# Kernel tuning notes

Measured on AMD Instinct MI355X. Metric: run time of the kernel, lower is better.

Reference implementation:

```python
import jax, jax.numpy as jnp
import numpy as np

N_USERS = 100000
N_GAMES = 20000
D_USER = 128
D_GAME = 64
EMB = 64
H = 256
E = 1000000
S = 500000


def setup_inputs() -> dict:
    key = jax.random.key(0)
    ks = jax.random.split(key, 32)

    def w(k, fi, fo):
        return jax.random.normal(k, (fi, fo), jnp.float32) / np.float32(np.sqrt(fi))

    d_game_full = D_GAME + EMB  # game features concat game embedding
    inp = {
        "x_user": jax.random.normal(ks[0], (N_USERS, D_USER), jnp.float32),
        "x_game": jax.random.normal(ks[1], (N_GAMES, D_GAME), jnp.float32),
        "emb_game": jax.random.normal(ks[2], (N_GAMES, EMB), jnp.float32) * 0.1,
        "edge_weight_ug": jax.random.uniform(ks[3], (E,), jnp.float32),
        "edge_weight_gu": jax.random.uniform(ks[4], (E,), jnp.float32),
        "src_ug": jax.random.randint(ks[5], (E,), 0, N_USERS, jnp.int32),
        "dst_ug": jax.random.randint(ks[6], (E,), 0, N_GAMES, jnp.int32),
        "src_gu": jax.random.randint(ks[7], (E,), 0, N_GAMES, jnp.int32),
        "dst_gu": jax.random.randint(ks[8], (E,), 0, N_USERS, jnp.int32),
        "score_row": jax.random.randint(ks[9], (S,), 0, N_USERS, jnp.int32),
        "score_col": jax.random.randint(ks[10], (S,), 0, N_GAMES, jnp.int32),
    }
    # GraphConv params per layer per edge type: W_rel (messages), bias, W_root (self)
    dims = [(D_USER, d_game_full, H), (H, H, H), (H, H, H)]
    i = 11
    for l, (du, dg, out) in enumerate(dims, 1):
        inp[f"W_rel_ug{l}"] = w(ks[i], du, out); i += 1
        inp[f"b_ug{l}"] = jnp.zeros((out,), jnp.float32)
        inp[f"W_root_g{l}"] = w(ks[i], dg, out); i += 1
        inp[f"W_rel_gu{l}"] = w(ks[i], dg, out); i += 1
        inp[f"b_gu{l}"] = jnp.zeros((out,), jnp.float32)
        inp[f"W_root_u{l}"] = w(ks[i], du, out); i += 1
    return inp


def reference(x_user, x_game, emb_game, edge_weight_ug, edge_weight_gu,
              W_rel_ug1, b_ug1, W_root_g1, W_rel_gu1, b_gu1, W_root_u1,
              W_rel_ug2, b_ug2, W_root_g2, W_rel_gu2, b_gu2, W_root_u2,
              W_rel_ug3, b_ug3, W_root_g3, W_rel_gu3, b_gu3, W_root_u3,
              src_ug, dst_ug, src_gu, dst_gu, score_row, score_col):
    def conv(x_src, x_dst, src, dst, ew, Wr, br, Wo, n_dst):
        # GraphConv: sum_j w_ij * x_j -> lin_rel, plus lin_root(x_i)
        msg = jax.ops.segment_sum(x_src[src] * ew[:, None], dst, num_segments=n_dst)
        return msg @ Wr + br + x_dst @ Wo

    xu = x_user                                   # [Nu, 128]
    xg = jnp.concatenate([x_game, emb_game], axis=1)  # [Ng, 128]

    g = jax.nn.relu(conv(xu, xg, src_ug, dst_ug, edge_weight_ug, W_rel_ug1, b_ug1, W_root_g1, N_GAMES))
    u = jax.nn.relu(conv(xg, xu, src_gu, dst_gu, edge_weight_gu, W_rel_gu1, b_gu1, W_root_u1, N_USERS))

    g2 = jax.nn.relu(conv(u, g, src_ug, dst_ug, edge_weight_ug, W_rel_ug2, b_ug2, W_root_g2, N_GAMES))
    u2 = jax.nn.relu(conv(g, u, src_gu, dst_gu, edge_weight_gu, W_rel_gu2, b_gu2, W_root_u2, N_USERS))

    g3 = conv(u2, g2, src_ug, dst_ug, edge_weight_ug, W_rel_ug3, b_ug3, W_root_g3, N_GAMES)
    u3 = conv(g2, u2, src_gu, dst_gu, edge_weight_gu, W_rel_gu3, b_gu3, W_root_u3, N_USERS)
    # dropout(0.2) in eval mode is identity

    # DotProductEdgeDecoder
    return jnp.sum(u3[score_row] * g3[score_col], axis=1)  # [S]
```

## Files before the change

kernel.cpp:

```cpp
#include <hip/hip_runtime.h>

typedef unsigned short bf16_t;
typedef __attribute__((ext_vector_type(8))) short bf16x8;
typedef __attribute__((ext_vector_type(4))) float f32x4;

static constexpr int NU = 100000;
static constexpr int NG = 20000;
static constexpr int HD = 256;
static constexpr int EE = 1000000;
static constexpr int SS = 500000;

static constexpr int SPAN = 1024;
static constexpr int BKT_G = (NG + SPAN - 1) / SPAN;
static constexpr int BKT_U = (NU + SPAN - 1) / SPAN;
static constexpr int PA_BLOCKS = 128;
static constexpr int PA_CHUNK = (EE + PA_BLOCKS - 1) / PA_BLOCKS;
static constexpr int TILE = 4096;

__device__ __forceinline__ float b2f(bf16_t u) {
    union { unsigned int i; float f; } x; x.i = ((unsigned int)u) << 16; return x.f;
}
__device__ __forceinline__ bf16_t f2b(float f) {
    union { float f; unsigned int i; } x; x.f = f;
    unsigned int r = x.i + 0x7FFF + ((x.i >> 16) & 1);
    return (bf16_t)(r >> 16);
}

__device__ __forceinline__ void accum8(float* acc, uint4 r, float w) {
    unsigned int u[4] = {r.x, r.y, r.z, r.w};
#pragma unroll
    for (int i = 0; i < 4; i++) {
        float lo = __uint_as_float(u[i] << 16);
        float hi = __uint_as_float(u[i] & 0xFFFF0000u);
        acc[2 * i]     = fmaf(w, lo, acc[2 * i]);
        acc[2 * i + 1] = fmaf(w, hi, acc[2 * i + 1]);
    }
}

__global__ void prep_feats(const float* __restrict__ xgame, const float* __restrict__ emb,
                           const float* __restrict__ xuser,
                           bf16_t* __restrict__ xg, bf16_t* __restrict__ xu,
                           int* __restrict__ gcg, int* __restrict__ gcu) {
    int id = blockIdx.x * 256 + threadIdx.x;
    if (id < BKT_G) gcg[id] = 0;
    if (id < BKT_U) gcu[id] = 0;
    const int ng4 = NG * 32;
    if (id < ng4) {
        int r = id >> 5, c = (id & 31) * 4;
        float4 v = (c < 64) ? *(const float4*)&xgame[(size_t)r * 64 + c]
                            : *(const float4*)&emb[(size_t)r * 64 + (c - 64)];
        ((ushort4*)xg)[id] = make_ushort4(f2b(v.x), f2b(v.y), f2b(v.z), f2b(v.w));
    } else {
        int j = id - ng4;
        if (j >= NU * 32) return;
        float4 v = ((const float4*)xuser)[j];
        ((ushort4*)xu)[j] = make_ushort4(f2b(v.x), f2b(v.y), f2b(v.z), f2b(v.w));
    }
}

struct WtArgs {
    const float* src[12];
    bf16_t* dst[12];
    int K[12];
    int off[13];
};
__global__ void wt_all(WtArgs a, int total) {
    int id = blockIdx.x * 256 + threadIdx.x;
    if (id >= total) return;
    int s = 0;
    while (id >= a.off[s + 1]) ++s;
    int local = id - a.off[s];
    int K = a.K[s];
    int k = local >> 8, n = local & 255;
    a.dst[s][(size_t)n * K + k] = f2b(a.src[s][local]);
}

__global__ __launch_bounds__(256) void chisto(const int* __restrict__ dug,
                                              const int* __restrict__ dgu,
                                              int* __restrict__ gcg, int* __restrict__ gcu) {
    __shared__ int cnt[128];
    int blk = blockIdx.x;
    int dir = blk >> 7, lb = blk & 127;
    const int* dst = dir ? dgu : dug;
    int* gc = dir ? gcu : gcg;
    int B = dir ? BKT_U : BKT_G;
    int t = threadIdx.x;
    if (t < 128) cnt[t] = 0;
    __syncthreads();
    int beg = lb * PA_CHUNK, fin = min(EE, beg + PA_CHUNK);
    for (int i = beg + t; i < fin; i += 256)
        atomicAdd(&cnt[((unsigned)dst[i]) >> 10], 1);
    __syncthreads();
    if (t < B && cnt[t]) atomicAdd(&gc[t], cnt[t]);
}

__global__ void scan_coarse(const int* __restrict__ gcg, const int* __restrict__ gcu,
                            int* __restrict__ baseg, int* __restrict__ baseu,
                            int* __restrict__ gcurg, int* __restrict__ gcuru,
                            int* __restrict__ rpg, int* __restrict__ rpu) {
    if (blockIdx.x == 0 && threadIdx.x == 0) {
        int run = 0;
        for (int i = 0; i < BKT_G; i++) { baseg[i] = run; gcurg[i] = run; run += gcg[i]; }
        rpg[NG] = EE;
    } else if (blockIdx.x == 1 && threadIdx.x == 0) {
        int run = 0;
        for (int i = 0; i < BKT_U; i++) { baseu[i] = run; gcuru[i] = run; run += gcu[i]; }
        rpu[NU] = EE;
    }
}

__global__ __launch_bounds__(256) void passA(
    const int* __restrict__ sug, const int* __restrict__ dug, const float* __restrict__ wug,
    const int* __restrict__ sgu, const int* __restrict__ dgu, const float* __restrict__ wgu,
    int* __restrict__ gcurg, int* __restrict__ gcuru,
    int2* __restrict__ tmpG, int2* __restrict__ tmpU) {
    __shared__ int cnt[128], sscan[128], gb[128];
    __shared__ unsigned short rankArr[TILE];
    __shared__ unsigned char sbkt[TILE];
    __shared__ int2 staged[TILE];
    int blk = blockIdx.x;
    int dir = blk >> 7, lb = blk & 127;
    const int* src = dir ? sgu : sug;
    const int* dst = dir ? dgu : dug;
    const float* w = dir ? wgu : wug;
    int* gcur = dir ? gcuru : gcurg;
    int2* tmp = dir ? tmpU : tmpG;
    int B = dir ? BKT_U : BKT_G;
    int t = threadIdx.x;
    int beg = lb * PA_CHUNK, fin = min(EE, beg + PA_CHUNK);
    for (int tb = beg; tb < fin; tb += TILE) {
        int n = min(TILE, fin - tb);
        if (t < 128) cnt[t] = 0;
        __syncthreads();
        for (int i = t; i < n; i += 256) {
            int bkt = ((unsigned)dst[tb + i]) >> 10;
            rankArr[i] = (unsigned short)atomicAdd(&cnt[bkt], 1);
        }
        __syncthreads();
        if (t == 0) {
            int run = 0;
            for (int i = 0; i < 128; i++) { sscan[i] = run; run += cnt[i]; }
        }
        __syncthreads();
        for (int i = t; i < n; i += 256) {
            unsigned d = (unsigned)dst[tb + i];
            int bkt = d >> 10;
            int pos = sscan[bkt] + rankArr[i];
            staged[pos] = make_int2(src[tb + i] | ((d & 1023u) << 17), __float_as_int(w[tb + i]));
            sbkt[pos] = (unsigned char)bkt;
        }
        __syncthreads();
        if (t < B && cnt[t]) gb[t] = atomicAdd(&gcur[t], cnt[t]);
        __syncthreads();
        for (int i = t; i < n; i += 256) {
            int bkt = sbkt[i];
            tmp[gb[bkt] + i - sscan[bkt]] = staged[i];
        }
        __syncthreads();
    }
}

__global__ __launch_bounds__(256) void passB(
    const int2* __restrict__ tmpG, const int2* __restrict__ tmpU,
    const int* __restrict__ baseg, const int* __restrict__ baseu,
    int* __restrict__ rpg, int* __restrict__ rpu,
    int2* __restrict__ eug, int2* __restrict__ egu) {
    __shared__ int hist[SPAN], excl[SPAN], sd[256];
    int b = blockIdx.x;
    const int2* tmp; const int* base; int* rowptr; int2* eout; int bkt, B, ntot;
    if (b < BKT_G) { tmp = tmpG; base = baseg; rowptr = rpg; eout = eug; bkt = b; B = BKT_G; ntot = NG; }
    else           { tmp = tmpU; base = baseu; rowptr = rpu; eout = egu; bkt = b - BKT_G; B = BKT_U; ntot = NU; }
    int start = base[bkt];
    int end = (bkt == B - 1) ? EE : base[bkt + 1];
    int row0 = bkt * SPAN;
    int t = threadIdx.x;
    for (int i = t; i < SPAN; i += 256) hist[i] = 0;
    __syncthreads();
    for (int i = start + t; i < end; i += 256)
        atomicAdd(&hist[((unsigned)tmp[i].x) >> 17], 1);
    __syncthreads();
    int v[4]; int s = 0;
#pragma unroll
    for (int j = 0; j < 4; j++) { v[j] = hist[t * 4 + j]; s += v[j]; }
    sd[t] = s;
    __syncthreads();
    for (int off = 1; off < 256; off <<= 1) {
        int y = (t >= off) ? sd[t - off] : 0;
        __syncthreads();
        sd[t] += y;
        __syncthreads();
    }
    int run = sd[t] - s;
#pragma unroll
    for (int j = 0; j < 4; j++) { excl[t * 4 + j] = run; run += v[j]; }
    __syncthreads();
    for (int r = t; r < SPAN; r += 256) {
        int row = row0 + r;
        if (row < ntot) rowptr[row] = start + excl[r];
    }
    for (int i = t; i < SPAN; i += 256) hist[i] = 0;
    __syncthreads();
    for (int i = start + t; i < end; i += 256) {
        int2 e = tmp[i];
        int dl = ((unsigned)e.x) >> 17;
        int pos = start + excl[dl] + atomicAdd(&hist[dl], 1);
        eout[pos] = make_int2(e.x & 0x1FFFF, e.y);
    }
}

template <int D>
__global__ __launch_bounds__(256) void seg_sum16(
    const bf16_t* __restrict__ feat, const int* __restrict__ rowptr,
    const int2* __restrict__ edges, bf16_t* __restrict__ out, int n_rows) {
    constexpr int LPE = D / 8;
    constexpr int EP = 64 / LPE;
    constexpr int UN = 4;
    int wid = (blockIdx.x * 256 + threadIdx.x) >> 6;
    int lane = threadIdx.x & 63;
    if (wid >= n_rows) return;
    int beg = rowptr[wid], end = rowptr[wid + 1];
    const int h = lane / LPE;
    const int cl = lane % LPE;
    const uint4* fb = (const uint4*)feat;
    float acc[8] = {};
    for (int eb = beg; eb < end; eb += UN * EP) {
        int2 ed[UN]; bool v[UN]; uint4 r[UN];
#pragma unroll
        for (int u = 0; u < UN; u++) {
            int e = eb + u * EP + h;
            v[u] = e < end;
            ed[u] = edges[v[u] ? e : beg];
        }
#pragma unroll
        for (int u = 0; u < UN; u++)
            r[u] = fb[(size_t)ed[u].x * (D / 8) + cl];
#pragma unroll
        for (int u = 0; u < UN; u++)
            accum8(acc, r[u], v[u] ? __int_as_float(ed[u].y) : 0.f);
    }
#pragma unroll
    for (int k = 0; k < 8; ++k) {
        acc[k] += __shfl_down(acc[k], 32, 64);
        if (LPE == 16) acc[k] += __shfl_down(acc[k], 16, 64);
    }
    if (lane < LPE) {
        uint4 o;
        o.x = (unsigned)f2b(acc[0]) | ((unsigned)f2b(acc[1]) << 16);
        o.y = (unsigned)f2b(acc[2]) | ((unsigned)f2b(acc[3]) << 16);
        o.z = (unsigned)f2b(acc[4]) | ((unsigned)f2b(acc[5]) << 16);
        o.w = (unsigned)f2b(acc[6]) | ((unsigned)f2b(acc[7]) << 16);
        ((uint4*)(out + (size_t)wid * D))[lane] = o;
    }
}

template <bool TWOPASS>
__global__ __launch_bounds__(256) void gemm_mfma(
    const bf16_t* __restrict__ A1, const bf16_t* __restrict__ W1t,
    const bf16_t* __restrict__ A2, const bf16_t* __restrict__ W2t,
    const float* __restrict__ bias, bf16_t* __restrict__ C,
    int M, int K, int addc, int relu) {
    constexpr int LS = 40;
    __shared__ bf16_t As[128 * LS];
    __shared__ bf16_t Bs[128 * LS];
    const int t = threadIdx.x;
    const int lane = t & 63, wave = t >> 6;
    const int wm = (wave >> 1) * 64, wn = (wave & 1) * 64;
    const int rowBase = blockIdx.x * 128;
    const int colBase = blockIdx.y * 128;
    const int lm = lane & 15;
    const int quad = lane >> 4;
    f32x4 acc[4][4] = {};

    const int npass = TWOPASS ? 2 : 1;
    for (int pass = 0; pass < npass; ++pass) {
        const bf16_t* A = pass ? A2 : A1;
        const bf16_t* Wt = pass ? W2t : W1t;
        for (int k0 = 0; k0 < K; k0 += 32) {
#pragma unroll
            for (int i = 0; i < 2; ++i) {
                int li = t + i * 256;
                int r = li >> 2, c = (li & 3) * 8;
                int gm = rowBase + r;
                bf16x8 v = {};
                if (gm < M) v = *(const bf16x8*)&A[(size_t)gm * K + k0 + c];
                *(bf16x8*)&As[r * LS + c] = v;
            }
#pragma unroll
            for (int i = 0; i < 2; ++i) {
                int li = t + i * 256;
                int r = li >> 2, c = (li & 3) * 8;
                bf16x8 v = *(const bf16x8*)&Wt[(size_t)(colBase + r) * K + k0 + c];
                *(bf16x8*)&Bs[r * LS + c] = v;
            }
            __syncthreads();
            bf16x8 af[4], bfr[4];
#pragma unroll
            for (int i = 0; i < 4; ++i)
                af[i] = *(const bf16x8*)&As[(wm + i * 16 + lm) * LS + quad * 8];
#pragma unroll
            for (int j = 0; j < 4; ++j)
                bfr[j] = *(const bf16x8*)&Bs[(wn + j * 16 + lm) * LS + quad * 8];
#pragma unroll
            for (int i = 0; i < 4; ++i)
#pragma unroll
                for (int j = 0; j < 4; ++j)
                    acc[i][j] = __builtin_amdgcn_mfma_f32_16x16x32_bf16(af[i], bfr[j], acc[i][j], 0, 0, 0);
            __syncthreads();
        }
    }

#pragma unroll
    for (int j = 0; j < 4; ++j) {
        int col = colBase + wn + j * 16 + lm;
        float bj = bias ? bias[col] : 0.f;
#pragma unroll
        for (int i = 0; i < 4; ++i) {
            int row0 = rowBase + wm + i * 16 + quad * 4;
#pragma unroll
            for (int r = 0; r < 4; ++r) {
                int row = row0 + r;
                if (row >= M) continue;
                float v = acc[i][j][r] + bj;
                bf16_t* cp = &C[(size_t)row * HD + col];
                if (addc) v += b2f(*cp);
                if (relu) v = fmaxf(v, 0.f);
                *cp = f2b(v);
            }
        }
    }
}

__global__ __launch_bounds__(256) void decode2(
    const bf16_t* __restrict__ u3, const bf16_t* __restrict__ g3,
    const int* __restrict__ row, const int* __restrict__ col,
    float* __restrict__ out, int S) {
    int wid = (blockIdx.x * 256 + threadIdx.x) >> 6;
    int lane = threadIdx.x & 63;
    int p = wid * 2 + (lane >> 5);
    int cl = lane & 31;
    if (p >= S) p = S - 1;
    int r = row[p], c = col[p];
    uint4 a = ((const uint4*)(u3 + (size_t)r * 256))[cl];
    uint4 b = ((const uint4*)(g3 + (size_t)c * 256))[cl];
    float s = 0.f;
    unsigned ua[4] = {a.x, a.y, a.z, a.w}, ub[4] = {b.x, b.y, b.z, b.w};
#pragma unroll
    for (int i = 0; i < 4; i++) {
        float alo = __uint_as_float(ua[i] << 16), ahi = __uint_as_float(ua[i] & 0xFFFF0000u);
        float blo = __uint_as_float(ub[i] << 16), bhi = __uint_as_float(ub[i] & 0xFFFF0000u);
        s = fmaf(alo, blo, s);
        s = fmaf(ahi, bhi, s);
    }
#pragma unroll
    for (int d = 16; d > 0; d >>= 1) s += __shfl_down(s, d, 64);
    if (cl == 0) out[p] = s;
}

extern "C" void kernel_launch(void* const* d_in, const int* in_sizes, int n_in,
                              void* d_out, int out_size, void* d_ws, size_t ws_size,
                              hipStream_t stream) {
    const float* x_user  = (const float*)d_in[0];
    const float* x_game  = (const float*)d_in[1];
    const float* emb_game= (const float*)d_in[2];
    const float* ew_ug   = (const float*)d_in[3];
    const float* ew_gu   = (const float*)d_in[4];
    const int* src_ug    = (const int*)d_in[5];
    const int* dst_ug    = (const int*)d_in[6];
    const int* src_gu    = (const int*)d_in[7];
    const int* dst_gu    = (const int*)d_in[8];
    const int* score_row = (const int*)d_in[9];
    const int* score_col = (const int*)d_in[10];
    const float* Wr_ug[3] = {(const float*)d_in[11], (const float*)d_in[17], (const float*)d_in[23]};
    const float* b_ug[3]  = {(const float*)d_in[12], (const float*)d_in[18], (const float*)d_in[24]};
    const float* Wo_g[3]  = {(const float*)d_in[13], (const float*)d_in[19], (const float*)d_in[25]};
    const float* Wr_gu[3] = {(const float*)d_in[14], (const float*)d_in[20], (const float*)d_in[26]};
    const float* b_gu[3]  = {(const float*)d_in[15], (const float*)d_in[21], (const float*)d_in[27]};
    const float* Wo_u[3]  = {(const float*)d_in[16], (const float*)d_in[22], (const float*)d_in[28]};
    float* out = (float*)d_out;
    (void)in_sizes; (void)n_in; (void)out_size;

    constexpr size_t WS_NEEDED = 183500000;
    if (ws_size < WS_NEEDED) return;

    char* ws = (char*)d_ws;
    size_t off = 0;
    auto alloc = [&](size_t bytes) -> void* {
        void* p = ws + off;
        off += (bytes + 255) & ~(size_t)255;
        return p;
    };
    bf16_t* xg   = (bf16_t*)alloc((size_t)NG * 128 * 2);
    bf16_t* xu   = (bf16_t*)alloc((size_t)NU * 128 * 2);
    bf16_t* uA   = (bf16_t*)alloc((size_t)NU * HD * 2);
    bf16_t* uB   = (bf16_t*)alloc((size_t)NU * HD * 2);
    bf16_t* gA   = (bf16_t*)alloc((size_t)NG * HD * 2);
    bf16_t* gB   = (bf16_t*)alloc((size_t)NG * HD * 2);
    bf16_t* buf  = (bf16_t*)alloc((size_t)NG * HD * 2);
    int2*   e_ug = (int2*)  alloc((size_t)EE * 8);
    int2*   e_gu = (int2*)  alloc((size_t)EE * 8);
    bf16_t* WrugT[3], *WogT[3], *WrguT[3], *WouT[3];
    const int Ks[3] = {128, 256, 256};
    for (int l = 0; l < 3; ++l) {
        WrugT[l] = (bf16_t*)alloc((size_t)Ks[l] * HD * 2);
        WogT[l]  = (bf16_t*)alloc((size_t)Ks[l] * HD * 2);
        WrguT[l] = (bf16_t*)alloc((size_t)Ks[l] * HD * 2);
        WouT[l]  = (bf16_t*)alloc((size_t)Ks[l] * HD * 2);
    }
    int* rowptr_g = (int*)alloc((NG + 1) * 4);
    int* rowptr_u = (int*)alloc((NU + 1) * 4);
    int* gcnt_g   = (int*)alloc(BKT_G * 4);
    int* gcnt_u   = (int*)alloc(BKT_U * 4);
    int* base_g   = (int*)alloc(BKT_G * 4);
    int* base_u   = (int*)alloc(BKT_U * 4);
    int* gcur_g   = (int*)alloc(BKT_G * 4);
    int* gcur_u   = (int*)alloc(BKT_U * 4);
    int2* tmp_g = (int2*)uB;
    int2* tmp_u = tmp_g + EE;

    {
        int n4 = NG * 32 + NU * 32;
        prep_feats<<<(n4 + 255) / 256, 256, 0, stream>>>(x_game, emb_game, x_user, xg, xu,
                                                         gcnt_g, gcnt_u);
        WtArgs wa;
        const float* srcs[12] = {Wr_ug[0], Wo_g[0], Wr_gu[0], Wo_u[0],
                                 Wr_ug[1], Wo_g[1], Wr_gu[1], Wo_u[1],
                                 Wr_ug[2], Wo_g[2], Wr_gu[2], Wo_u[2]};
        bf16_t* dsts[12] = {WrugT[0], WogT[0], WrguT[0], WouT[0],
                            WrugT[1], WogT[1], WrguT[1], WouT[1],
                            WrugT[2], WogT[2], WrguT[2], WouT[2]};
        int total = 0;
        for (int i = 0; i < 12; ++i) {
            wa.src[i] = srcs[i]; wa.dst[i] = dsts[i];
            wa.K[i] = Ks[i / 4]; wa.off[i] = total;
            total += Ks[i / 4] * HD;
        }
        wa.off[12] = total;
        wt_all<<<(total + 255) / 256, 256, 0, stream>>>(wa, total);
    }
    chisto<<<2 * PA_BLOCKS, 256, 0, stream>>>(dst_ug, dst_gu, gcnt_g, gcnt_u);
    scan_coarse<<<2, 64, 0, stream>>>(gcnt_g, gcnt_u, base_g, base_u, gcur_g, gcur_u,
                                      rowptr_g, rowptr_u);
    passA<<<2 * PA_BLOCKS, 256, 0, stream>>>(src_ug, dst_ug, ew_ug, src_gu, dst_gu, ew_gu,
                                             gcur_g, gcur_u, tmp_g, tmp_u);
    passB<<<BKT_G + BKT_U, 256, 0, stream>>>(tmp_g, tmp_u, base_g, base_u,
                                             rowptr_g, rowptr_u, e_ug, e_gu);

    const dim3 GG((NG + 127) / 128, 2), GU((NU + 127) / 128, 2);
    const int SEG_G = (NG + 3) / 4, SEG_U = (NU + 3) / 4;

    seg_sum16<128><<<SEG_G, 256, 0, stream>>>(xu, rowptr_g, e_ug, buf, NG);
    gemm_mfma<true><<<GG, 256, 0, stream>>>(buf, WrugT[0], xg, WogT[0], b_ug[0], gA, NG, 128, 0, 1);
    gemm_mfma<false><<<GG, 256, 0, stream>>>(xg, WrguT[0], nullptr, nullptr, nullptr, buf, NG, 128, 0, 0);
    seg_sum16<256><<<SEG_U, 256, 0, stream>>>(buf, rowptr_u, e_gu, uA, NU);
    gemm_mfma<false><<<GU, 256, 0, stream>>>(xu, WouT[0], nullptr, nullptr, b_gu[0], uA, NU, 128, 1, 1);

    seg_sum16<256><<<SEG_G, 256, 0, stream>>>(uA, rowptr_g, e_ug, buf, NG);
    gemm_mfma<true><<<GG, 256, 0, stream>>>(buf, WrugT[1], gA, WogT[1], b_ug[1], gB, NG, 256, 0, 1);
    gemm_mfma<false><<<GG, 256, 0, stream>>>(gA, WrguT[1], nullptr, nullptr, nullptr, buf, NG, 256, 0, 0);
    seg_sum16<256><<<SEG_U, 256, 0, stream>>>(buf, rowptr_u, e_gu, uB, NU);
    gemm_mfma<false><<<GU, 256, 0, stream>>>(uA, WouT[1], nullptr, nullptr, b_gu[1], uB, NU, 256, 1, 1);

    seg_sum16<256><<<SEG_G, 256, 0, stream>>>(uB, rowptr_g, e_ug, buf, NG);
    gemm_mfma<true><<<GG, 256, 0, stream>>>(buf, WrugT[2], gB, WogT[2], b_ug[2], gA, NG, 256, 0, 0);
    gemm_mfma<false><<<GG, 256, 0, stream>>>(gB, WrguT[2], nullptr, nullptr, nullptr, buf, NG, 256, 0, 0);
    seg_sum16<256><<<SEG_U, 256, 0, stream>>>(buf, rowptr_u, e_gu, uA, NU);
    gemm_mfma<false><<<GU, 256, 0, stream>>>(uB, WouT[2], nullptr, nullptr, b_gu[2], uA, NU, 256, 1, 0);

    decode2<<<((SS + 1) / 2 + 3) / 4, 256, 0, stream>>>(uA, gA, score_row, score_col, out, SS);
}
```

Baseline: 1.128 ms.

## Split CSR fine-sort pass into sliced histogram, global scan, and atomic scatter

The per-bucket fine sort, which ran one block per 1024-row bucket (118 blocks total), is replaced by a sliced global-histogram pass (8 blocks per bucket), a three-kernel global prefix scan over per-row counts, and a scatter pass that uses global atomics on per-row cursors. The coarse pass block count is also doubled. The aim is more parallelism in the CSR build, paid for with extra kernel launches, global atomics and additional count and cursor arrays. Edge order within a row becomes nondeterministic, which can change the summation order.

New measurement: 1.100 ms. -2.5%, faster.

```diff
diff --git a/kernel.cpp b/kernel.cpp
--- a/kernel.cpp
+++ b/kernel.cpp
@@ -13,9 +13,11 @@
 static constexpr int SPAN = 1024;
 static constexpr int BKT_G = (NG + SPAN - 1) / SPAN;
 static constexpr int BKT_U = (NU + SPAN - 1) / SPAN;
-static constexpr int PA_BLOCKS = 128;
+static constexpr int PA_BLOCKS = 256;
 static constexpr int PA_CHUNK = (EE + PA_BLOCKS - 1) / PA_BLOCKS;
 static constexpr int TILE = 4096;
+static constexpr int NSC_G = (NG + 1023) / 1024;
+static constexpr int NSC_U = (NU + 1023) / 1024;
 
 __device__ __forceinline__ float b2f(bf16_t u) {
     union { unsigned int i; float f; } x; x.i = ((unsigned int)u) << 16; return x.f;
@@ -77,10 +79,14 @@
 
 __global__ __launch_bounds__(256) void chisto(const int* __restrict__ dug,
                                               const int* __restrict__ dgu,
-                                              int* __restrict__ gcg, int* __restrict__ gcu) {
+                                              int* __restrict__ gcg, int* __restrict__ gcu,
+                                              int* __restrict__ rcg, int* __restrict__ rcu) {
     __shared__ int cnt[128];
     int blk = blockIdx.x;
-    int dir = blk >> 7, lb = blk & 127;
+    int gid = blk * 256 + threadIdx.x;
+    if (gid < NG) rcg[gid] = 0;
+    else if (gid < NG + NU) rcu[gid - NG] = 0;
+    int dir = blk >> 8, lb = blk & 255;
     const int* dst = dir ? dgu : dug;
     int* gc = dir ? gcu : gcg;
     int B = dir ? BKT_U : BKT_G;
@@ -119,7 +125,7 @@
     __shared__ unsigned char sbkt[TILE];
     __shared__ int2 staged[TILE];
     int blk = blockIdx.x;
-    int dir = blk >> 7, lb = blk & 127;
+    int dir = blk >> 8, lb = blk & 255;
     const int* src = dir ? sgu : sug;
     const int* dst = dir ? dgu : dug;
     const float* w = dir ? wgu : wug;
@@ -160,28 +166,50 @@
     }
 }
 
-__global__ __launch_bounds__(256) void passB(
+__device__ __forceinline__ void slice_bounds(const int* base, int bkt, int B, int sl,
+                                             int& s0, int& s1) {
+    int start = base[bkt];
+    int end = (bkt == B - 1) ? EE : base[bkt + 1];
+    int len = end - start;
+    s0 = start + (int)(((long long)len * sl) >> 3);
+    s1 = start + (int)(((long long)len * (sl + 1)) >> 3);
+}
+
+__global__ __launch_bounds__(256) void passB_hist(
     const int2* __restrict__ tmpG, const int2* __restrict__ tmpU,
     const int* __restrict__ baseg, const int* __restrict__ baseu,
-    int* __restrict__ rpg, int* __restrict__ rpu,
-    int2* __restrict__ eug, int2* __restrict__ egu) {
-    __shared__ int hist[SPAN], excl[SPAN], sd[256];
-    int b = blockIdx.x;
-    const int2* tmp; const int* base; int* rowptr; int2* eout; int bkt, B, ntot;
-    if (b < BKT_G) { tmp = tmpG; base = baseg; rowptr = rpg; eout = eug; bkt = b; B = BKT_G; ntot = NG; }
-    else           { tmp = tmpU; base = baseu; rowptr = rpu; eout = egu; bkt = b - BKT_G; B = BKT_U; ntot = NU; }
-    int start = base[bkt];
-    int end = (bkt == B - 1) ? EE : base[bkt + 1];
-    int row0 = bkt * SPAN;
+    int* __restrict__ rcg, int* __restrict__ rcu) {
+    __shared__ int hist[SPAN];
+    int b = blockIdx.x >> 3, sl = blockIdx.x & 7;
+    const int2* tmp; const int* base; int* rowcnt; int bkt, B;
+    if (b < BKT_G) { tmp = tmpG; base = baseg; rowcnt = rcg; bkt = b; B = BKT_G; }
+    else           { tmp = tmpU; base = baseu; rowcnt = rcu; bkt = b - BKT_G; B = BKT_U; }
+    int s0, s1;
+    slice_bounds(base, bkt, B, sl, s0, s1);
     int t = threadIdx.x;
     for (int i = t; i < SPAN; i += 256) hist[i] = 0;
     __syncthreads();
-    for (int i = start + t; i < end; i += 256)
+    for (int i = s0 + t; i < s1; i += 256)
         atomicAdd(&hist[((unsigned)tmp[i].x) >> 17], 1);
     __syncthreads();
+    int row0 = bkt * SPAN;
+    for (int i = t; i < SPAN; i += 256)
+        if (hist[i]) atomicAdd(&rowcnt[row0 + i], hist[i]);
+}
+
+__device__ __forceinline__ void scan1_body(const int* cnt, int* rowptr, int* bsum,
+                                           int* cur, int n, int lb) {
+    __shared__ int sd[256];
+    int t = threadIdx.x;
+    int base = lb * 1024;
     int v[4]; int s = 0;
 #pragma unroll
-    for (int j = 0; j < 4; j++) { v[j] = hist[t * 4 + j]; s += v[j]; }
+    for (int i = 0; i < 4; i++) {
+        int idx = base + t * 4 + i;
+        v[i] = (idx < n) ? cnt[idx] : 0;
+        if (idx < n) cur[idx] = 0;
+        s += v[i];
+    }
     sd[t] = s;
     __syncthreads();
     for (int off = 1; off < 256; off <<= 1) {
@@ -192,18 +220,74 @@
     }
     int run = sd[t] - s;
 #pragma unroll
-    for (int j = 0; j < 4; j++) { excl[t * 4 + j] = run; run += v[j]; }
-    __syncthreads();
-    for (int r = t; r < SPAN; r += 256) {
-        int row = row0 + r;
-        if (row < ntot) rowptr[row] = start + excl[r];
-    }
-    for (int i = t; i < SPAN; i += 256) hist[i] = 0;
-    __syncthreads();
-    for (int i = start + t; i < end; i += 256) {
+    for (int i = 0; i < 4; i++) {
+        int idx = base + t * 4 + i;
+        if (idx < n) rowptr[idx] = run;
+        run += v[i];
+    }
+    if (t == 255) bsum[lb] = sd[255];
+}
+
+__global__ void scan1b(const int* __restrict__ cg, int* __restrict__ rpg, int* __restrict__ bsg,
+                       int* __restrict__ curg,
+                       const int* __restrict__ cu, int* __restrict__ rpu, int* __restrict__ bsu,
+                       int* __restrict__ curu) {
+    int b = blockIdx.x;
+    if (b < NSC_G) scan1_body(cg, rpg, bsg, curg, NG, b);
+    else           scan1_body(cu, rpu, bsu, curu, NU, b - NSC_G);
+}
+
+__global__ void scan2b(int* __restrict__ bsg, int* __restrict__ bsu) {
+    if (blockIdx.x != 0) return;
+    if (threadIdx.x == 0) {
+        int run = 0;
+        for (int i = 0; i < NSC_G; i++) { int v = bsg[i]; bsg[i] = run; run += v; }
+    } else if (threadIdx.x == 1) {
+        int run = 0;
+        for (int i = 0; i < NSC_U; i++) { int v = bsu[i]; bsu[i] = run; run += v; }
+    }
+}
+
+__global__ void scan3b(int* __restrict__ rpg, const int* __restrict__ bsg,
+                       int* __restrict__ rpu, const int* __restrict__ bsu) {
+    int b = blockIdx.x;
+    int t = threadIdx.x;
+    if (b < NSC_G) {
+        int add = bsg[b];
+        int base = b * 1024;
+#pragma unroll
+        for (int i = 0; i < 4; i++) {
+            int idx = base + t * 4 + i;
+            if (idx < NG) rpg[idx] += add;
+        }
+    } else {
+        int add = bsu[b - NSC_G];
+        int base = (b - NSC_G) * 1024;
+#pragma unroll
+        for (int i = 0; i < 4; i++) {
+            int idx = base + t * 4 + i;
+            if (idx < NU) rpu[idx] += add;
+        }
+    }
+}
+
+__global__ __launch_bounds__(256) void passB_scat(
+    const int2* __restrict__ tmpG, const int2* __restrict__ tmpU,
+    const int* __restrict__ baseg, const int* __restrict__ baseu,
+    const int* __restrict__ rpg, const int* __restrict__ rpu,
+    int* __restrict__ curg, int* __restrict__ curu,
+    int2* __restrict__ eug, int2* __restrict__ egu) {
+    int b = blockIdx.x >> 3, sl = blockIdx.x & 7;
+    const int2* tmp; const int* base; const int* rowptr; int* cur; int2* eout; int bkt, B;
+    if (b < BKT_G) { tmp = tmpG; base = baseg; rowptr = rpg; cur = curg; eout = eug; bkt = b; B = BKT_G; }
+    else           { tmp = tmpU; base = baseu; rowptr = rpu; cur = curu; eout = egu; bkt = b - BKT_G; B = BKT_U; }
+    int s0, s1;
+    slice_bounds(base, bkt, B, sl, s0, s1);
+    int row0 = bkt * SPAN;
+    for (int i = s0 + threadIdx.x; i < s1; i += 256) {
         int2 e = tmp[i];
-        int dl = ((unsigned)e.x) >> 17;
-        int pos = start + excl[dl] + atomicAdd(&hist[dl], 1);
+        int row = row0 + (int)(((unsigned)e.x) >> 17);
+        int pos = rowptr[row] + atomicAdd(&cur[row], 1);
         eout[pos] = make_int2(e.x & 0x1FFFF, e.y);
     }
 }
@@ -408,12 +492,18 @@
     }
     int* rowptr_g = (int*)alloc((NG + 1) * 4);
     int* rowptr_u = (int*)alloc((NU + 1) * 4);
+    int* rowcnt_g = (int*)alloc(NG * 4);
+    int* rowcnt_u = (int*)alloc(NU * 4);
+    int* rowcur_g = (int*)alloc(NG * 4);
+    int* rowcur_u = (int*)alloc(NU * 4);
     int* gcnt_g   = (int*)alloc(BKT_G * 4);
     int* gcnt_u   = (int*)alloc(BKT_U * 4);
     int* base_g   = (int*)alloc(BKT_G * 4);
     int* base_u   = (int*)alloc(BKT_U * 4);
     int* gcur_g   = (int*)alloc(BKT_G * 4);
     int* gcur_u   = (int*)alloc(BKT_U * 4);
+    int* bsum_g   = (int*)alloc(NSC_G * 4);
+    int* bsum_u   = (int*)alloc(NSC_U * 4);
     int2* tmp_g = (int2*)uB;
     int2* tmp_u = tmp_g + EE;
 
@@ -437,13 +527,21 @@
         wa.off[12] = total;
         wt_all<<<(total + 255) / 256, 256, 0, stream>>>(wa, total);
     }
-    chisto<<<2 * PA_BLOCKS, 256, 0, stream>>>(dst_ug, dst_gu, gcnt_g, gcnt_u);
+    chisto<<<2 * PA_BLOCKS, 256, 0, stream>>>(dst_ug, dst_gu, gcnt_g, gcnt_u,
+                                              rowcnt_g, rowcnt_u);
     scan_coarse<<<2, 64, 0, stream>>>(gcnt_g, gcnt_u, base_g, base_u, gcur_g, gcur_u,
                                       rowptr_g, rowptr_u);
     passA<<<2 * PA_BLOCKS, 256, 0, stream>>>(src_ug, dst_ug, ew_ug, src_gu, dst_gu, ew_gu,
                                              gcur_g, gcur_u, tmp_g, tmp_u);
-    passB<<<BKT_G + BKT_U, 256, 0, stream>>>(tmp_g, tmp_u, base_g, base_u,
-                                             rowptr_g, rowptr_u, e_ug, e_gu);
+    passB_hist<<<(BKT_G + BKT_U) * 8, 256, 0, stream>>>(tmp_g, tmp_u, base_g, base_u,
+                                                        rowcnt_g, rowcnt_u);
+    scan1b<<<NSC_G + NSC_U, 256, 0, stream>>>(rowcnt_g, rowptr_g, bsum_g, rowcur_g,
+                                              rowcnt_u, rowptr_u, bsum_u, rowcur_u);
+    scan2b<<<1, 64, 0, stream>>>(bsum_g, bsum_u);
+    scan3b<<<NSC_G + NSC_U, 256, 0, stream>>>(rowptr_g, bsum_g, rowptr_u, bsum_u);
+    passB_scat<<<(BKT_G + BKT_U) * 8, 256, 0, stream>>>(tmp_g, tmp_u, base_g, base_u,
+                                                        rowptr_g, rowptr_u,
+                                                        rowcur_g, rowcur_u, e_ug, e_gu);
 
     const dim3 GG((NG + 127) / 128, 2), GU((NU + 127) / 128, 2);
     const int SEG_G = (NG + 3) / 4, SEG_U = (NU + 3) / 4;
```

## Use finer CSR buckets with staged LDS sort and vectorized GEMM epilogue

Applied to the files above, without the earlier changes.

The two-pass counting sort that builds CSR moves from 1024-row buckets to 64-row (games) and 128-row (users) buckets. passA now takes a single tile per block with a parallel scan, and passB stages each bucket in LDS so the output is written coalesced, with a chunked fallback for oversized buckets. This gives many more, smaller passB blocks in place of a few large ones with global scatter. The GEMM swaps the MFMA operand order so each lane holds four consecutive columns, which allows vectorized bias, residual and store in the epilogue. It adds more buckets for the serial scan_coarse to walk, and passB keeps a thread-0 serial scan per bucket.

Measured after the change: 931.7 us. 17.4% less time.

```diff
diff --git a/kernel.cpp b/kernel.cpp
--- a/kernel.cpp
+++ b/kernel.cpp
@@ -10,10 +10,14 @@
 static constexpr int EE = 1000000;
 static constexpr int SS = 500000;
 
-static constexpr int SPAN = 1024;
-static constexpr int BKT_G = (NG + SPAN - 1) / SPAN;
-static constexpr int BKT_U = (NU + SPAN - 1) / SPAN;
-static constexpr int PA_BLOCKS = 128;
+static constexpr int SH_G = 6,  SPAN_G = 64;
+static constexpr int SH_U = 7,  SPAN_U = 128;
+static constexpr int BKT_G = (NG + SPAN_G - 1) / SPAN_G;
+static constexpr int BKT_U = (NU + SPAN_U - 1) / SPAN_U;
+static constexpr int CAP_G = 4096;
+static constexpr int CAP_U = 2048;
+static constexpr int NBMAX = 1024;
+static constexpr int PA_BLOCKS = 256;
 static constexpr int PA_CHUNK = (EE + PA_BLOCKS - 1) / PA_BLOCKS;
 static constexpr int TILE = 4096;
 
@@ -78,20 +82,22 @@
 __global__ __launch_bounds__(256) void chisto(const int* __restrict__ dug,
                                               const int* __restrict__ dgu,
                                               int* __restrict__ gcg, int* __restrict__ gcu) {
-    __shared__ int cnt[128];
+    __shared__ int cnt[NBMAX];
     int blk = blockIdx.x;
-    int dir = blk >> 7, lb = blk & 127;
+    int dir = blk >> 8, lb = blk & 255;
     const int* dst = dir ? dgu : dug;
     int* gc = dir ? gcu : gcg;
     int B = dir ? BKT_U : BKT_G;
+    int sh = dir ? SH_U : SH_G;
     int t = threadIdx.x;
-    if (t < 128) cnt[t] = 0;
+    for (int i = t; i < NBMAX; i += 256) cnt[i] = 0;
     __syncthreads();
     int beg = lb * PA_CHUNK, fin = min(EE, beg + PA_CHUNK);
     for (int i = beg + t; i < fin; i += 256)
-        atomicAdd(&cnt[((unsigned)dst[i]) >> 10], 1);
-    __syncthreads();
-    if (t < B && cnt[t]) atomicAdd(&gc[t], cnt[t]);
+        atomicAdd(&cnt[((unsigned)dst[i]) >> sh], 1);
+    __syncthreads();
+    for (int i = t; i < B; i += 256)
+        if (cnt[i]) atomicAdd(&gc[i], cnt[i]);
 }
 
 __global__ void scan_coarse(const int* __restrict__ gcg, const int* __restrict__ gcu,
@@ -114,97 +120,166 @@
     const int* __restrict__ sgu, const int* __restrict__ dgu, const float* __restrict__ wgu,
     int* __restrict__ gcurg, int* __restrict__ gcuru,
     int2* __restrict__ tmpG, int2* __restrict__ tmpU) {
-    __shared__ int cnt[128], sscan[128], gb[128];
-    __shared__ unsigned short rankArr[TILE];
-    __shared__ unsigned char sbkt[TILE];
+    __shared__ int cnt[NBMAX], sscan[NBMAX], gb[NBMAX], sd[256];
+    __shared__ unsigned short rankArr[TILE], sbkt[TILE];
     __shared__ int2 staged[TILE];
     int blk = blockIdx.x;
-    int dir = blk >> 7, lb = blk & 127;
+    int dir = blk >> 8, lb = blk & 255;
     const int* src = dir ? sgu : sug;
     const int* dst = dir ? dgu : dug;
     const float* w = dir ? wgu : wug;
     int* gcur = dir ? gcuru : gcurg;
     int2* tmp = dir ? tmpU : tmpG;
     int B = dir ? BKT_U : BKT_G;
+    int sh = dir ? SH_U : SH_G;
+    unsigned lmask = dir ? (SPAN_U - 1) : (SPAN_G - 1);
     int t = threadIdx.x;
     int beg = lb * PA_CHUNK, fin = min(EE, beg + PA_CHUNK);
-    for (int tb = beg; tb < fin; tb += TILE) {
-        int n = min(TILE, fin - tb);
-        if (t < 128) cnt[t] = 0;
-        __syncthreads();
-        for (int i = t; i < n; i += 256) {
-            int bkt = ((unsigned)dst[tb + i]) >> 10;
-            rankArr[i] = (unsigned short)atomicAdd(&cnt[bkt], 1);
+    int n = fin - beg;
+    for (int i = t; i < NBMAX; i += 256) cnt[i] = 0;
+    __syncthreads();
+    for (int i = t; i < n; i += 256) {
+        int bkt = ((unsigned)dst[beg + i]) >> sh;
+        rankArr[i] = (unsigned short)atomicAdd(&cnt[bkt], 1);
+    }
+    __syncthreads();
+    {
+        int v[4]; int s = 0;
+#pragma unroll
+        for (int j = 0; j < 4; j++) { v[j] = cnt[t * 4 + j]; s += v[j]; }
+        sd[t] = s;
+        __syncthreads();
+        for (int off = 1; off < 256; off <<= 1) {
+            int y = (t >= off) ? sd[t - off] : 0;
+            __syncthreads();
+            sd[t] += y;
+            __syncthreads();
+        }
+        int run = sd[t] - s;
+#pragma unroll
+        for (int j = 0; j < 4; j++) { sscan[t * 4 + j] = run; run += v[j]; }
+    }
+    __syncthreads();
+    for (int i = t; i < n; i += 256) {
+        unsigned d = (unsigned)dst[beg + i];
+        int bkt = d >> sh;
+        int pos = sscan[bkt] + rankArr[i];
+        staged[pos] = make_int2(src[beg + i] | ((d & lmask) << 17), __float_as_int(w[beg + i]));
+        sbkt[pos] = (unsigned short)bkt;
+    }
+    __syncthreads();
+    for (int i = t; i < B; i += 256)
+        if (cnt[i]) gb[i] = atomicAdd(&gcur[i], cnt[i]);
+    __syncthreads();
+    for (int i = t; i < n; i += 256) {
+        int bkt = sbkt[i];
+        tmp[gb[bkt] + i - sscan[bkt]] = staged[i];
+    }
+}
+
+template <int SPANB, int CAP>
+__global__ __launch_bounds__(256) void passB(
+    const int2* __restrict__ tmp, const int* __restrict__ base,
+    int* __restrict__ rowptr, int2* __restrict__ eout, int B, int ntot) {
+    __shared__ int cnt2[SPANB], lexcl[SPANB], cur[SPANB];
+    __shared__ int2 staged[CAP];
+    constexpr int KMAX = CAP / 256;
+    int bkt = blockIdx.x;
+    if (bkt >= B) return;
+    int start = base[bkt];
+    int end = (bkt == B - 1) ? EE : base[bkt + 1];
+    int row0 = bkt * SPANB;
+    int t = threadIdx.x;
+    int count = end - start;
+    if (count <= CAP) {
+        for (int i = t; i < SPANB; i += 256) cnt2[i] = 0;
+        __syncthreads();
+        int2 e[KMAX]; int rk[KMAX];
+#pragma unroll
+        for (int k = 0; k < KMAX; k++) {
+            int i = t + k * 256;
+            if (i < count) {
+                e[k] = tmp[start + i];
+                rk[k] = atomicAdd(&cnt2[((unsigned)e[k].x) >> 17], 1);
+            }
         }
         __syncthreads();
         if (t == 0) {
             int run = 0;
-            for (int i = 0; i < 128; i++) { sscan[i] = run; run += cnt[i]; }
-        }
-        __syncthreads();
-        for (int i = t; i < n; i += 256) {
-            unsigned d = (unsigned)dst[tb + i];
-            int bkt = d >> 10;
-            int pos = sscan[bkt] + rankArr[i];
-            staged[pos] = make_int2(src[tb + i] | ((d & 1023u) << 17), __float_as_int(w[tb + i]));
-            sbkt[pos] = (unsigned char)bkt;
-        }
-        __syncthreads();
-        if (t < B && cnt[t]) gb[t] = atomicAdd(&gcur[t], cnt[t]);
-        __syncthreads();
-        for (int i = t; i < n; i += 256) {
-            int bkt = sbkt[i];
-            tmp[gb[bkt] + i - sscan[bkt]] = staged[i];
-        }
-        __syncthreads();
-    }
-}
-
-__global__ __launch_bounds__(256) void passB(
-    const int2* __restrict__ tmpG, const int2* __restrict__ tmpU,
-    const int* __restrict__ baseg, const int* __restrict__ baseu,
-    int* __restrict__ rpg, int* __restrict__ rpu,
-    int2* __restrict__ eug, int2* __restrict__ egu) {
-    __shared__ int hist[SPAN], excl[SPAN], sd[256];
-    int b = blockIdx.x;
-    const int2* tmp; const int* base; int* rowptr; int2* eout; int bkt, B, ntot;
-    if (b < BKT_G) { tmp = tmpG; base = baseg; rowptr = rpg; eout = eug; bkt = b; B = BKT_G; ntot = NG; }
-    else           { tmp = tmpU; base = baseu; rowptr = rpu; eout = egu; bkt = b - BKT_G; B = BKT_U; ntot = NU; }
-    int start = base[bkt];
-    int end = (bkt == B - 1) ? EE : base[bkt + 1];
-    int row0 = bkt * SPAN;
-    int t = threadIdx.x;
-    for (int i = t; i < SPAN; i += 256) hist[i] = 0;
-    __syncthreads();
-    for (int i = start + t; i < end; i += 256)
-        atomicAdd(&hist[((unsigned)tmp[i].x) >> 17], 1);
-    __syncthreads();
-    int v[4]; int s = 0;
-#pragma unroll
-    for (int j = 0; j < 4; j++) { v[j] = hist[t * 4 + j]; s += v[j]; }
-    sd[t] = s;
-    __syncthreads();
-    for (int off = 1; off < 256; off <<= 1) {
-        int y = (t >= off) ? sd[t - off] : 0;
-        __syncthreads();
-        sd[t] += y;
-        __syncthreads();
-    }
-    int run = sd[t] - s;
-#pragma unroll
-    for (int j = 0; j < 4; j++) { excl[t * 4 + j] = run; run += v[j]; }
-    __syncthreads();
-    for (int r = t; r < SPAN; r += 256) {
-        int row = row0 + r;
-        if (row < ntot) rowptr[row] = start + excl[r];
-    }
-    for (int i = t; i < SPAN; i += 256) hist[i] = 0;
-    __syncthreads();
-    for (int i = start + t; i < end; i += 256) {
-        int2 e = tmp[i];
-        int dl = ((unsigned)e.x) >> 17;
-        int pos = start + excl[dl] + atomicAdd(&hist[dl], 1);
-        eout[pos] = make_int2(e.x & 0x1FFFF, e.y);
+            for (int r = 0; r < SPANB; r++) { lexcl[r] = run; run += cnt2[r]; }
+        }
+        __syncthreads();
+#pragma unroll
+        for (int k = 0; k < KMAX; k++) {
+            int i = t + k * 256;
+            if (i < count) {
+                int r = ((unsigned)e[k].x) >> 17;
+                staged[lexcl[r] + rk[k]] = e[k];
+            }
+        }
+        __syncthreads();
+        for (int r = t; r < SPANB; r += 256) {
+            int row = row0 + r;
+            if (row < ntot) rowptr[row] = start + lexcl[r];
+        }
+        for (int i = t; i < count; i += 256) {
+            int2 s = staged[i];
+            eout[start + i] = make_int2(s.x & 0x1FFFF, s.y);
+        }
+    } else {
+        for (int i = t; i < SPANB; i += 256) cnt2[i] = 0;
+        __syncthreads();
+        for (int i = start + t; i < end; i += 256)
+            atomicAdd(&cnt2[((unsigned)tmp[i].x) >> 17], 1);
+        __syncthreads();
+        if (t == 0) {
+            int run = 0;
+            for (int r = 0; r < SPANB; r++) { int v = cnt2[r]; cur[r] = run; run += v; }
+        }
+        __syncthreads();
+        for (int r = t; r < SPANB; r += 256) {
+            int row = row0 + r;
+            if (row < ntot) rowptr[row] = start + cur[r];
+        }
+        __syncthreads();
+        for (int pos = start; pos < end; pos += CAP) {
+            int n = min(CAP, end - pos);
+            for (int i = t; i < SPANB; i += 256) cnt2[i] = 0;
+            __syncthreads();
+            int2 e[KMAX]; int rk[KMAX];
+#pragma unroll
+            for (int k = 0; k < KMAX; k++) {
+                int i = t + k * 256;
+                if (i < n) {
+                    e[k] = tmp[pos + i];
+                    rk[k] = atomicAdd(&cnt2[((unsigned)e[k].x) >> 17], 1);
+                }
+            }
+            __syncthreads();
+            if (t == 0) {
+                int run = 0;
+                for (int r = 0; r < SPANB; r++) { lexcl[r] = run; run += cnt2[r]; }
+            }
+            __syncthreads();
+#pragma unroll
+            for (int k = 0; k < KMAX; k++) {
+                int i = t + k * 256;
+                if (i < n) {
+                    int r = ((unsigned)e[k].x) >> 17;
+                    staged[lexcl[r] + rk[k]] = e[k];
+                }
+            }
+            __syncthreads();
+            for (int i = t; i < n; i += 256) {
+                int2 s = staged[i];
+                int r = ((unsigned)s.x) >> 17;
+                int g = start + cur[r] + (i - lexcl[r]);
+                eout[g] = make_int2(s.x & 0x1FFFF, s.y);
+            }
+            __syncthreads();
+            for (int r = t; r < SPANB; r += 256) cur[r] += cnt2[r];
+            __syncthreads();
+        }
     }
 }
 
@@ -304,28 +379,33 @@
             for (int i = 0; i < 4; ++i)
 #pragma unroll
                 for (int j = 0; j < 4; ++j)
-                    acc[i][j] = __builtin_amdgcn_mfma_f32_16x16x32_bf16(af[i], bfr[j], acc[i][j], 0, 0, 0);
-            __syncthreads();
-        }
-    }
-
-#pragma unroll
-    for (int j = 0; j < 4; ++j) {
-        int col = colBase + wn + j * 16 + lm;
-        float bj = bias ? bias[col] : 0.f;
-#pragma unroll
-        for (int i = 0; i < 4; ++i) {
-            int row0 = rowBase + wm + i * 16 + quad * 4;
-#pragma unroll
-            for (int r = 0; r < 4; ++r) {
-                int row = row0 + r;
-                if (row >= M) continue;
-                float v = acc[i][j][r] + bj;
-                bf16_t* cp = &C[(size_t)row * HD + col];
-                if (addc) v += b2f(*cp);
-                if (relu) v = fmaxf(v, 0.f);
-                *cp = f2b(v);
-            }
+                    acc[i][j] = __builtin_amdgcn_mfma_f32_16x16x32_bf16(bfr[j], af[i], acc[i][j], 0, 0, 0);
+            __syncthreads();
+        }
+    }
+
+#pragma unroll
+    for (int i = 0; i < 4; ++i) {
+        int row = rowBase + wm + i * 16 + lm;
+        if (row >= M) continue;
+#pragma unroll
+        for (int j = 0; j < 4; ++j) {
+            int col = colBase + wn + j * 16 + quad * 4;
+            float v0 = acc[i][j][0], v1 = acc[i][j][1], v2 = acc[i][j][2], v3 = acc[i][j][3];
+            if (bias) {
+                float4 b4 = *(const float4*)&bias[col];
+                v0 += b4.x; v1 += b4.y; v2 += b4.z; v3 += b4.w;
+            }
+            bf16_t* cp = &C[(size_t)row * HD + col];
+            if (addc) {
+                ushort4 old = *(const ushort4*)cp;
+                v0 += b2f(old.x); v1 += b2f(old.y); v2 += b2f(old.z); v3 += b2f(old.w);
+            }
+            if (relu) {
+                v0 = fmaxf(v0, 0.f); v1 = fmaxf(v1, 0.f);
+                v2 = fmaxf(v2, 0.f); v3 = fmaxf(v3, 0.f);
+            }
+            *(ushort4*)cp = make_ushort4(f2b(v0), f2b(v1), f2b(v2), f2b(v3));
         }
     }
 }
@@ -442,8 +522,8 @@
                                       rowptr_g, rowptr_u);
     passA<<<2 * PA_BLOCKS, 256, 0, stream>>>(src_ug, dst_ug, ew_ug, src_gu, dst_gu, ew_gu,
                                              gcur_g, gcur_u, tmp_g, tmp_u);
-    passB<<<BKT_G + BKT_U, 256, 0, stream>>>(tmp_g, tmp_u, base_g, base_u,
-                                             rowptr_g, rowptr_u, e_ug, e_gu);
+    passB<SPAN_G, CAP_G><<<BKT_G, 256, 0, stream>>>(tmp_g, base_g, rowptr_g, e_ug, BKT_G, NG);
+    passB<SPAN_U, CAP_U><<<BKT_U, 256, 0, stream>>>(tmp_u, base_u, rowptr_u, e_gu, BKT_U, NU);
 
     const dim3 GG((NG + 127) / 128, 2), GU((NU + 127) / 128, 2);
     const int SEG_G = (NG + 3) / 4, SEG_U = (NU + 3) / 4;
```
